# Kernel tuning notes

Measured on AMD Instinct MI355X. Metric: run time of the kernel, lower is better.

Reference implementation:

```python
import jax, jax.numpy as jnp
import numpy as np

ALPHA = 0.2  # LeakyReLU negative slope


def setup_inputs() -> dict:
    key = jax.random.key(0)
    k1, k2, k3, k4, k5 = jax.random.split(key, 5)
    N, H, W, T, V, F = 8, 64, 64, 32, 32, 32
    h = jax.random.normal(k1, (N, H, W, T, V), dtype=jnp.float32)
    W_map = jax.random.normal(k2, (T, F), dtype=jnp.float32) * (1.414 / np.sqrt(T))
    b_map = jax.random.normal(k3, (F,), dtype=jnp.float32) * 0.01
    a_attn = jax.random.normal(k4, (2 * F, 1), dtype=jnp.float32) * (1.414 / np.sqrt(2 * F))
    B_adj = jax.random.normal(k5, (V, V), dtype=jnp.float32) * 1e-3 + 1e-6
    return {"h": h, "W_map": W_map, "b_map": b_map, "a_attn": a_attn, "B_adj": B_adj}


def reference(h, W_map, b_map, a_attn, B_adj):
    # h: (N,H,W,T,V) -> (N,V,H,W,T)
    hv = jnp.transpose(h, (0, 4, 1, 2, 3))
    Wh = hv @ W_map + b_map  # (N,V,H,W,F) -- LinearMapping
    N, V, H, W, F = Wh.shape
    # pairwise concat + matmul with a decomposes exactly into two projections
    a1, a2 = a_attn[:F, 0], a_attn[F:, 0]
    e = (jnp.einsum('nihwf,f->nihw', Wh, a1)[:, :, None, :, :]
         + jnp.einsum('njhwf,f->njhw', Wh, a2)[:, None, :, :, :])  # (N,V,V,H,W)
    e = jnp.where(e > 0, e, ALPHA * e)  # LeakyReLU
    attn = jax.nn.softmax(e, axis=-1)  # softmax over the W dim (as in original: dim=-1 of (N,V,V,H,W))
    # normalized adjacency: (B + I), min-max scaled, symmetric degree normalization
    adj = B_adj + jnp.eye(V, dtype=B_adj.dtype)
    adj = (adj - adj.min()) / (adj.max() - adj.min())
    d12 = 1.0 / jnp.sqrt(jnp.sum(adj, axis=1))
    adj_n = d12[:, None] * adj * d12[None, :]  # (V,V)
    # weighted aggregation over source vertices j (the original double for-loop)
    hp = jnp.einsum('nijhw,njhwf->inhwf', attn, Wh)  # (V,N,H,W,F)
    # replicate permute(1,3,4,2,0).view(N,H,W*F,V) @ adj_n
    hp = jnp.transpose(hp, (1, 3, 4, 2, 0)).reshape(N, H, W * F, V)
    hp = (hp @ adj_n).reshape(N, H, W, F, V)
    return jax.nn.elu(hp)
```

## Files before the change

kernel.cpp:

```cpp
#include <hip/hip_runtime.h>
#include <math.h>

typedef __attribute__((ext_vector_type(8))) short bf16x8;
typedef __attribute__((ext_vector_type(16))) float f32x16;
typedef __attribute__((ext_vector_type(4))) float f32x4;

static constexpr size_t WS_WA   = 0;
static constexpr size_t WS_C12  = 64;
static constexpr size_t WS_WMF  = 96;
static constexpr size_t WS_ADJF = 608;

__device__ __forceinline__ unsigned short f2bf(float x){
    union { float f; unsigned u; } c; c.f = x;
    unsigned r = c.u + 0x7FFFu + ((c.u >> 16) & 1u);
    return (unsigned short)(r >> 16);
}
__device__ __forceinline__ unsigned pk2(float a, float b){
    return (unsigned)f2bf(a) | ((unsigned)f2bf(b) << 16);
}
__device__ __forceinline__ float bf2f(unsigned short v){
    return __uint_as_float(((unsigned)v) << 16);
}
__device__ __forceinline__ float elu(float x){ return x > 0.f ? x : __expf(x) - 1.0f; }
__device__ __forceinline__ float lrelu(float x){ return fmaxf(x, 0.2f * x); }

__global__ __launch_bounds__(1024) void k0_prep(const float* __restrict__ W_map,
    const float* __restrict__ b_map, const float* __restrict__ a_attn,
    const float* __restrict__ B_adj, float* __restrict__ ws)
{
    __shared__ float lds[1024];
    __shared__ float d12[32];
    int tid = threadIdx.x;
    int i = tid >> 5, j = tid & 31;
    float a = B_adj[tid] + (i == j ? 1.0f : 0.0f);
    lds[tid] = a; __syncthreads();
    for (int s = 512; s > 0; s >>= 1) { if (tid < s) lds[tid] = fmaxf(lds[tid], lds[tid + s]); __syncthreads(); }
    float mx = lds[0]; __syncthreads();
    lds[tid] = a; __syncthreads();
    for (int s = 512; s > 0; s >>= 1) { if (tid < s) lds[tid] = fminf(lds[tid], lds[tid + s]); __syncthreads(); }
    float mn = lds[0]; __syncthreads();
    lds[tid] = (a - mn) / (mx - mn); __syncthreads();
    if (tid < 32) {
        float s = 0.f;
        for (int jj = 0; jj < 32; ++jj) s += lds[tid * 32 + jj];
        d12[tid] = 1.0f / sqrtf(s);
    }
    __syncthreads();

    {
        int kap = tid >> 9, rem = tid & 511, l = rem >> 3, e = rem & 7;
        int krow = 16 * kap + 8 * (l >> 5) + e;
        int col  = l & 31;
        ((unsigned short*)(ws + WS_WMF))[tid] = f2bf(W_map[krow * 32 + col]);
        float aij = B_adj[krow * 32 + col] + (krow == col ? 1.0f : 0.0f);
        float adjv = d12[krow] * ((aij - mn) / (mx - mn)) * d12[col];
        ((unsigned short*)(ws + WS_ADJF))[tid] = f2bf(adjv);
    }
    if (tid < 32) {
        float w1 = 0.f, w2 = 0.f;
        for (int f = 0; f < 32; ++f) {
            w1 += W_map[tid * 32 + f] * a_attn[f];
            w2 += W_map[tid * 32 + f] * a_attn[32 + f];
        }
        ws[WS_WA + tid] = w1; ws[WS_WA + 32 + tid] = w2;
    }
    if (tid == 0) {
        float c1 = 0.f, c2 = 0.f;
        for (int f = 0; f < 32; ++f) { c1 += b_map[f] * a_attn[f]; c2 += b_map[f] * a_attn[32 + f]; }
        ws[WS_C12] = c1; ws[WS_C12 + 1] = c2;
    }
}

template<int KAP>
__device__ __forceinline__ bf16x8 xform(const f32x16& d, int hi){
    unsigned b0 = pk2(d[8*KAP+0], d[8*KAP+1]);
    unsigned b1 = pk2(d[8*KAP+2], d[8*KAP+3]);
    unsigned b2 = pk2(d[8*KAP+4], d[8*KAP+5]);
    unsigned b3 = pk2(d[8*KAP+6], d[8*KAP+7]);
    unsigned pb0 = (unsigned)__shfl_xor((int)b0, 32, 64);
    unsigned pb1 = (unsigned)__shfl_xor((int)b1, 32, 64);
    unsigned pb2 = (unsigned)__shfl_xor((int)b2, 32, 64);
    unsigned pb3 = (unsigned)__shfl_xor((int)b3, 32, 64);
    union { unsigned u[4]; bf16x8 v; } t;
    t.u[0] = hi ? pb2 : b0;
    t.u[1] = hi ? pb3 : b1;
    t.u[2] = hi ? b2 : pb0;
    t.u[3] = hi ? b3 : pb1;
    return t.v;
}

__global__ __launch_bounds__(1024) void kfused(const float* __restrict__ hin,
    const float* __restrict__ b_map, const float* __restrict__ ws, float* __restrict__ out)
{
    __shared__ unsigned short hbf[64 * 1024];
    __shared__ float s1L[64 * 32];
    __shared__ float s2L[64 * 32];
    __shared__ float rdenL[32 * 32];
    __shared__ float waL[64];

    const int tid = threadIdx.x;
    const int wv = tid >> 6, l = tid & 63;
    const int c = l & 31, hi = l >> 5;
    const int nh = blockIdx.x;
    const int hh = nh & 63, n = nh >> 6;

    if (tid < 64) waL[tid] = ws[WS_WA + tid];
    const float c1 = ws[WS_C12], c2 = ws[WS_C12 + 1];
    const float bc = b_map[c];

    bf16x8 B1f[2], B2f[2];
    {
        const unsigned short* wmf = (const unsigned short*)(ws + WS_WMF);
        const unsigned short* adf = (const unsigned short*)(ws + WS_ADJF);
        B1f[0] = *(const bf16x8*)(wmf + l * 8);
        B1f[1] = *(const bf16x8*)(wmf + 512 + l * 8);
        B2f[0] = *(const bf16x8*)(adf + l * 8);
        B2f[1] = *(const bf16x8*)(adf + 512 + l * 8);
    }

    {
        const float* hrow = hin + (long)nh * 65536;
        unsigned* hb32 = (unsigned*)hbf;
#pragma unroll
        for (int it = 0; it < 8; ++it) {
            int slot = it * 1024 + tid;
            int s = slot >> 7, r = slot & 127;
            int t = (r >> 3) * 2, v0 = (r & 7) * 4;
            f32x4 x0 = *(const f32x4*)(hrow + s * 1024 + t * 32 + v0);
            f32x4 x1 = *(const f32x4*)(hrow + s * 1024 + (t + 1) * 32 + v0);
            int kap = t >> 4, e = t & 7, lb = 32 * ((t >> 3) & 1);
#pragma unroll
            for (int cc = 0; cc < 4; ++cc) {
                int u16i = s * 1024 + kap * 512 + (v0 + cc + lb) * 8 + e;
                hb32[u16i >> 1] = pk2(x0[cc], x1[cc]);
            }
        }
    }
    __syncthreads();

    {
        float wa1v[16], wa2v[16];
#pragma unroll
        for (int kk = 0; kk < 16; ++kk) {
            int t = 16 * (kk >> 3) + 8 * hi + (kk & 7);
            wa1v[kk] = waL[t]; wa2v[kk] = waL[32 + t];
        }
#pragma unroll
        for (int k = 0; k < 4; ++k) {
            int s = wv * 4 + k;
            const unsigned short* fp = hbf + s * 1024;
            bf16x8 f0 = *(const bf16x8*)(fp + l * 8);
            bf16x8 f1 = *(const bf16x8*)(fp + 512 + l * 8);
            float p1 = 0.f, p2 = 0.f;
#pragma unroll
            for (int e = 0; e < 8; ++e) {
                float x = bf2f((unsigned short)f0[e]);
                p1 = fmaf(x, wa1v[e], p1); p2 = fmaf(x, wa2v[e], p2);
            }
#pragma unroll
            for (int e = 0; e < 8; ++e) {
                float x = bf2f((unsigned short)f1[e]);
                p1 = fmaf(x, wa1v[8 + e], p1); p2 = fmaf(x, wa2v[8 + e], p2);
            }
            p1 += __shfl_xor(p1, 32, 64);
            p2 += __shfl_xor(p2, 32, 64);
            if (!hi) { s1L[s * 32 + c] = p1 + c1; s2L[s * 32 + c] = p2 + c2; }
        }
    }
    __syncthreads();

    {
        int i = tid >> 5, j = tid & 31;
        float sum = 0.f;
#pragma unroll
        for (int w = 0; w < 64; ++w)
            sum += __expf(lrelu(s1L[w * 32 + i] + s2L[w * 32 + j]));
        rdenL[tid] = 1.0f / sum;
    }
    __syncthreads();

    const int hh5 = hh >> 5, f3 = hh & 31;
#pragma unroll 1
    for (int k = 0; k < 4; ++k) {
        const int s = wv * 4 + k;
        const unsigned short* fp = hbf + s * 1024;
        bf16x8 a10 = *(const bf16x8*)(fp + l * 8);
        bf16x8 a11 = *(const bf16x8*)(fp + 512 + l * 8);

        f32x16 d1;
#pragma unroll
        for (int r = 0; r < 16; ++r) d1[r] = bc;
        d1 = __builtin_amdgcn_mfma_f32_32x32x16_bf16(a10, B1f[0], d1, 0, 0, 0);
        d1 = __builtin_amdgcn_mfma_f32_32x32x16_bf16(a11, B1f[1], d1, 0, 0, 0);
        bf16x8 A3_0 = xform<0>(d1, hi);
        bf16x8 A3_1 = xform<1>(d1, hi);

        const float s2c = s2L[s * 32 + c];
        f32x4 sa = *(const f32x4*)&s1L[s * 32 + 8 * hi];
        f32x4 sb = *(const f32x4*)&s1L[s * 32 + 8 * hi + 4];
        f32x4 sc_ = *(const f32x4*)&s1L[s * 32 + 16 + 8 * hi];
        f32x4 sd = *(const f32x4*)&s1L[s * 32 + 16 + 8 * hi + 4];
        float q[16];
#pragma unroll
        for (int e = 0; e < 4; ++e) {
            int i0 = 8 * hi + e, i1 = 8 * hi + 4 + e, i2i = 16 + 8 * hi + e, i3 = 16 + 8 * hi + 4 + e;
            q[e]      = __expf(lrelu(sa[e] + s2c)) * rdenL[i0 * 32 + c];
            q[4 + e]  = __expf(lrelu(sb[e] + s2c)) * rdenL[i1 * 32 + c];
            q[8 + e]  = __expf(lrelu(sc_[e] + s2c)) * rdenL[i2i * 32 + c];
            q[12 + e] = __expf(lrelu(sd[e] + s2c)) * rdenL[i3 * 32 + c];
        }
        union { unsigned u[4]; bf16x8 v; } A2_0, A2_1;
        A2_0.u[0] = pk2(q[0], q[1]);  A2_0.u[1] = pk2(q[2], q[3]);
        A2_0.u[2] = pk2(q[4], q[5]);  A2_0.u[3] = pk2(q[6], q[7]);
        A2_1.u[0] = pk2(q[8], q[9]);  A2_1.u[1] = pk2(q[10], q[11]);
        A2_1.u[2] = pk2(q[12], q[13]); A2_1.u[3] = pk2(q[14], q[15]);

        f32x16 d2;
#pragma unroll
        for (int r = 0; r < 16; ++r) d2[r] = 0.f;
        d2 = __builtin_amdgcn_mfma_f32_32x32x16_bf16(A2_0.v, B2f[0], d2, 0, 0, 0);
        d2 = __builtin_amdgcn_mfma_f32_32x32x16_bf16(A2_1.v, B2f[1], d2, 0, 0, 0);
        bf16x8 B3_0 = xform<0>(d2, hi);
        bf16x8 B3_1 = xform<1>(d2, hi);

        f32x16 d3;
#pragma unroll
        for (int r = 0; r < 16; ++r) d3[r] = 0.f;
        d3 = __builtin_amdgcn_mfma_f32_32x32x16_bf16(A3_0, B3_0, d3, 0, 0, 0);
        d3 = __builtin_amdgcn_mfma_f32_32x32x16_bf16(A3_1, B3_1, d3, 0, 0, 0);

        float* ob = out + (((long)(n * 64 + s) * 64) * 32 + f3) * 32 + c;
#pragma unroll
        for (int r = 0; r < 16; ++r) {
            int f = (r & 3) + 8 * (r >> 2) + 4 * hi;
            ob[(f * 2 + hh5) * 1024] = elu(d3[r]);
        }
    }
}

extern "C" void kernel_launch(void* const* d_in, const int* in_sizes, int n_in,
                              void* d_out, int out_size, void* d_ws, size_t ws_size,
                              hipStream_t stream) {
    (void)in_sizes; (void)n_in; (void)out_size; (void)ws_size;
    const float* hin    = (const float*)d_in[0];
    const float* W_map  = (const float*)d_in[1];
    const float* b_map  = (const float*)d_in[2];
    const float* a_attn = (const float*)d_in[3];
    const float* B_adj  = (const float*)d_in[4];
    float* out = (float*)d_out;
    float* ws  = (float*)d_ws;

    hipLaunchKernelGGL(k0_prep, dim3(1),   dim3(1024), 0, stream, W_map, b_map, a_attn, B_adj, ws);
    hipLaunchKernelGGL(kfused,  dim3(512), dim3(1024), 0, stream, hin, b_map, ws, out);
}
```

Baseline: 70.68 us.

## Split fused kernel into score/denominator pass and finer-grained main pass

Moves the attention score projections and softmax denominators into a separate kernel that writes them to workspace. The main kernel then splits each (n,h) row across four smaller 512-thread blocks, each staging only its quarter of h in LDS. This cuts LDS use per block to raise occupancy. Output stores become nontemporal. The cost is reading h twice from global memory, plus an extra launch and a workspace round trip for the scores.

```diff
diff --git a/kernel.cpp b/kernel.cpp
--- a/kernel.cpp
+++ b/kernel.cpp
@@ -4,11 +4,15 @@
 typedef __attribute__((ext_vector_type(8))) short bf16x8;
 typedef __attribute__((ext_vector_type(16))) float f32x16;
 typedef __attribute__((ext_vector_type(4))) float f32x4;
+typedef __attribute__((ext_vector_type(8))) unsigned short us8;
 
 static constexpr size_t WS_WA   = 0;
 static constexpr size_t WS_C12  = 64;
 static constexpr size_t WS_WMF  = 96;
 static constexpr size_t WS_ADJF = 608;
+static constexpr size_t WS_S1   = 2048;
+static constexpr size_t WS_S2   = WS_S1 + (size_t)1048576;
+static constexpr size_t WS_DEN  = WS_S2 + (size_t)1048576;
 
 __device__ __forceinline__ unsigned short f2bf(float x){
     union { float f; unsigned u; } c; c.f = x;
@@ -17,9 +21,6 @@
 }
 __device__ __forceinline__ unsigned pk2(float a, float b){
     return (unsigned)f2bf(a) | ((unsigned)f2bf(b) << 16);
-}
-__device__ __forceinline__ float bf2f(unsigned short v){
-    return __uint_as_float(((unsigned)v) << 16);
 }
 __device__ __forceinline__ float elu(float x){ return x > 0.f ? x : __expf(x) - 1.0f; }
 __device__ __forceinline__ float lrelu(float x){ return fmaxf(x, 0.2f * x); }
@@ -71,6 +72,42 @@
     }
 }
 
+__global__ __launch_bounds__(1024) void k12(const float* __restrict__ hin, float* __restrict__ ws)
+{
+    __shared__ float s1L[64 * 32], s2L[64 * 32], waL[64];
+    const int tid = threadIdx.x;
+    if (tid < 64) waL[tid] = ws[WS_WA + tid];
+    const float c1 = ws[WS_C12], c2 = ws[WS_C12 + 1];
+    const long nh = blockIdx.x;
+    const float* hrow = hin + nh * 65536;
+    __syncthreads();
+
+    const int i = tid & 31, s0 = tid >> 5;
+#pragma unroll
+    for (int its = 0; its < 2; ++its) {
+        const int s = s0 + its * 32;
+        const float* hp = hrow + s * 1024;
+        float a1 = c1, a2 = c2;
+#pragma unroll
+        for (int t = 0; t < 32; ++t) {
+            float x = hp[t * 32 + i];
+            a1 = fmaf(x, waL[t], a1);
+            a2 = fmaf(x, waL[32 + t], a2);
+        }
+        s1L[s * 32 + i] = a1; s2L[s * 32 + i] = a2;
+        ws[WS_S1 + nh * 2048 + s * 32 + i] = a1;
+        ws[WS_S2 + nh * 2048 + s * 32 + i] = a2;
+    }
+    __syncthreads();
+
+    const int ii = tid >> 5, j = tid & 31;
+    float sum = 0.f;
+#pragma unroll
+    for (int w = 0; w < 64; ++w)
+        sum += __expf(lrelu(s1L[w * 32 + ii] + s2L[w * 32 + j]));
+    ws[WS_DEN + nh * 1024 + tid] = 1.0f / sum;
+}
+
 template<int KAP>
 __device__ __forceinline__ bf16x8 xform(const f32x16& d, int hi){
     unsigned b0 = pk2(d[8*KAP+0], d[8*KAP+1]);
@@ -89,24 +126,40 @@
     return t.v;
 }
 
-__global__ __launch_bounds__(1024) void kfused(const float* __restrict__ hin,
+__global__ __launch_bounds__(512, 4) void kmain(const float* __restrict__ hin,
     const float* __restrict__ b_map, const float* __restrict__ ws, float* __restrict__ out)
 {
-    __shared__ unsigned short hbf[64 * 1024];
-    __shared__ float s1L[64 * 32];
-    __shared__ float s2L[64 * 32];
-    __shared__ float rdenL[32 * 32];
-    __shared__ float waL[64];
+    __shared__ unsigned short hbf[16 * 1024];
+    __shared__ float rdenL[1024];
 
     const int tid = threadIdx.x;
     const int wv = tid >> 6, l = tid & 63;
     const int c = l & 31, hi = l >> 5;
-    const int nh = blockIdx.x;
-    const int hh = nh & 63, n = nh >> 6;
-
-    if (tid < 64) waL[tid] = ws[WS_WA + tid];
-    const float c1 = ws[WS_C12], c2 = ws[WS_C12 + 1];
-    const float bc = b_map[c];
+    const int blk = blockIdx.x;
+    const long nh = blk >> 2;
+    const int qr = blk & 3;
+    const int hh = (int)(nh & 63), n = (int)(nh >> 6);
+
+    rdenL[tid]       = ws[WS_DEN + nh * 1024 + tid];
+    rdenL[tid + 512] = ws[WS_DEN + nh * 1024 + tid + 512];
+
+    {
+        const float* hq = hin + nh * 65536 + qr * 16384;
+        const int v = tid & 31;
+#pragma unroll
+        for (int it = 0; it < 4; ++it) {
+            const int gid = (it * 512 + tid) >> 5;
+            const int site = gid >> 2, kap = (gid >> 1) & 1, hw = gid & 1;
+            const float* hp = hq + site * 1024 + (16 * kap + 8 * hw) * 32 + v;
+            float x[8];
+#pragma unroll
+            for (int e = 0; e < 8; ++e) x[e] = hp[e * 32];
+            union { unsigned u[4]; us8 v8; } pk;
+            pk.u[0] = pk2(x[0], x[1]); pk.u[1] = pk2(x[2], x[3]);
+            pk.u[2] = pk2(x[4], x[5]); pk.u[3] = pk2(x[6], x[7]);
+            *(us8*)(hbf + site * 1024 + kap * 512 + (v + 32 * hw) * 8) = pk.v8;
+        }
+    }
 
     bf16x8 B1f[2], B2f[2];
     {
@@ -117,73 +170,16 @@
         B2f[0] = *(const bf16x8*)(adf + l * 8);
         B2f[1] = *(const bf16x8*)(adf + 512 + l * 8);
     }
-
-    {
-        const float* hrow = hin + (long)nh * 65536;
-        unsigned* hb32 = (unsigned*)hbf;
-#pragma unroll
-        for (int it = 0; it < 8; ++it) {
-            int slot = it * 1024 + tid;
-            int s = slot >> 7, r = slot & 127;
-            int t = (r >> 3) * 2, v0 = (r & 7) * 4;
-            f32x4 x0 = *(const f32x4*)(hrow + s * 1024 + t * 32 + v0);
-            f32x4 x1 = *(const f32x4*)(hrow + s * 1024 + (t + 1) * 32 + v0);
-            int kap = t >> 4, e = t & 7, lb = 32 * ((t >> 3) & 1);
-#pragma unroll
-            for (int cc = 0; cc < 4; ++cc) {
-                int u16i = s * 1024 + kap * 512 + (v0 + cc + lb) * 8 + e;
-                hb32[u16i >> 1] = pk2(x0[cc], x1[cc]);
-            }
-        }
-    }
-    __syncthreads();
-
-    {
-        float wa1v[16], wa2v[16];
-#pragma unroll
-        for (int kk = 0; kk < 16; ++kk) {
-            int t = 16 * (kk >> 3) + 8 * hi + (kk & 7);
-            wa1v[kk] = waL[t]; wa2v[kk] = waL[32 + t];
-        }
-#pragma unroll
-        for (int k = 0; k < 4; ++k) {
-            int s = wv * 4 + k;
-            const unsigned short* fp = hbf + s * 1024;
-            bf16x8 f0 = *(const bf16x8*)(fp + l * 8);
-            bf16x8 f1 = *(const bf16x8*)(fp + 512 + l * 8);
-            float p1 = 0.f, p2 = 0.f;
-#pragma unroll
-            for (int e = 0; e < 8; ++e) {
-                float x = bf2f((unsigned short)f0[e]);
-                p1 = fmaf(x, wa1v[e], p1); p2 = fmaf(x, wa2v[e], p2);
-            }
-#pragma unroll
-            for (int e = 0; e < 8; ++e) {
-                float x = bf2f((unsigned short)f1[e]);
-                p1 = fmaf(x, wa1v[8 + e], p1); p2 = fmaf(x, wa2v[8 + e], p2);
-            }
-            p1 += __shfl_xor(p1, 32, 64);
-            p2 += __shfl_xor(p2, 32, 64);
-            if (!hi) { s1L[s * 32 + c] = p1 + c1; s2L[s * 32 + c] = p2 + c2; }
-        }
-    }
-    __syncthreads();
-
-    {
-        int i = tid >> 5, j = tid & 31;
-        float sum = 0.f;
-#pragma unroll
-        for (int w = 0; w < 64; ++w)
-            sum += __expf(lrelu(s1L[w * 32 + i] + s2L[w * 32 + j]));
-        rdenL[tid] = 1.0f / sum;
-    }
+    const float bc = b_map[c];
     __syncthreads();
 
     const int hh5 = hh >> 5, f3 = hh & 31;
 #pragma unroll 1
-    for (int k = 0; k < 4; ++k) {
-        const int s = wv * 4 + k;
-        const unsigned short* fp = hbf + s * 1024;
+    for (int k = 0; k < 2; ++k) {
+        const int ls = wv * 2 + k;
+        const int gw = qr * 16 + ls;
+        const long site = nh * 64 + gw;
+        const unsigned short* fp = hbf + ls * 1024;
         bf16x8 a10 = *(const bf16x8*)(fp + l * 8);
         bf16x8 a11 = *(const bf16x8*)(fp + 512 + l * 8);
 
@@ -195,11 +191,12 @@
         bf16x8 A3_0 = xform<0>(d1, hi);
         bf16x8 A3_1 = xform<1>(d1, hi);
 
-        const float s2c = s2L[s * 32 + c];
-        f32x4 sa = *(const f32x4*)&s1L[s * 32 + 8 * hi];
-        f32x4 sb = *(const f32x4*)&s1L[s * 32 + 8 * hi + 4];
-        f32x4 sc_ = *(const f32x4*)&s1L[s * 32 + 16 + 8 * hi];
-        f32x4 sd = *(const f32x4*)&s1L[s * 32 + 16 + 8 * hi + 4];
+        const float* s1p = ws + WS_S1 + site * 32;
+        const float s2c = ws[WS_S2 + site * 32 + c];
+        f32x4 sa  = *(const f32x4*)(s1p + 8 * hi);
+        f32x4 sb  = *(const f32x4*)(s1p + 8 * hi + 4);
+        f32x4 sc_ = *(const f32x4*)(s1p + 16 + 8 * hi);
+        f32x4 sd  = *(const f32x4*)(s1p + 16 + 8 * hi + 4);
         float q[16];
 #pragma unroll
         for (int e = 0; e < 4; ++e) {
@@ -210,9 +207,9 @@
             q[12 + e] = __expf(lrelu(sd[e] + s2c)) * rdenL[i3 * 32 + c];
         }
         union { unsigned u[4]; bf16x8 v; } A2_0, A2_1;
-        A2_0.u[0] = pk2(q[0], q[1]);  A2_0.u[1] = pk2(q[2], q[3]);
-        A2_0.u[2] = pk2(q[4], q[5]);  A2_0.u[3] = pk2(q[6], q[7]);
-        A2_1.u[0] = pk2(q[8], q[9]);  A2_1.u[1] = pk2(q[10], q[11]);
+        A2_0.u[0] = pk2(q[0], q[1]);   A2_0.u[1] = pk2(q[2], q[3]);
+        A2_0.u[2] = pk2(q[4], q[5]);   A2_0.u[3] = pk2(q[6], q[7]);
+        A2_1.u[0] = pk2(q[8], q[9]);   A2_1.u[1] = pk2(q[10], q[11]);
         A2_1.u[2] = pk2(q[12], q[13]); A2_1.u[3] = pk2(q[14], q[15]);
 
         f32x16 d2;
@@ -229,11 +226,11 @@
         d3 = __builtin_amdgcn_mfma_f32_32x32x16_bf16(A3_0, B3_0, d3, 0, 0, 0);
         d3 = __builtin_amdgcn_mfma_f32_32x32x16_bf16(A3_1, B3_1, d3, 0, 0, 0);
 
-        float* ob = out + (((long)(n * 64 + s) * 64) * 32 + f3) * 32 + c;
+        float* ob = out + (((long)(n * 64 + gw) * 64) * 32 + f3) * 32 + c;
 #pragma unroll
         for (int r = 0; r < 16; ++r) {
             int f = (r & 3) + 8 * (r >> 2) + 4 * hi;
-            ob[(f * 2 + hh5) * 1024] = elu(d3[r]);
+            __builtin_nontemporal_store(elu(d3[r]), ob + (f * 2 + hh5) * 1024);
         }
     }
 }
@@ -250,6 +247,7 @@
     float* out = (float*)d_out;
     float* ws  = (float*)d_ws;
 
-    hipLaunchKernelGGL(k0_prep, dim3(1),   dim3(1024), 0, stream, W_map, b_map, a_attn, B_adj, ws);
-    hipLaunchKernelGGL(kfused,  dim3(512), dim3(1024), 0, stream, hin, b_map, ws, out);
-}
+    hipLaunchKernelGGL(k0_prep, dim3(1),    dim3(1024), 0, stream, W_map, b_map, a_attn, B_adj, ws);
+    hipLaunchKernelGGL(k12,     dim3(512),  dim3(1024), 0, stream, hin, ws);
+    hipLaunchKernelGGL(kmain,   dim3(2048), dim3(512),  0, stream, hin, b_map, ws, out);
+}
```

Measured after the change: 86.83 us. 1.23x slower.
